# Kernel tuning notes

Hardware: AMD Instinct MI355X
Metric: run time of the kernel (lower is better)

Reference implementation:

```python
import jax, jax.numpy as jnp
import numpy as np

B, N, TASK_DIM, HW_DIM, EMB = 32768, 32, 17, 16, 64


def _w(key, shape, scale=0.1):
    return jax.random.normal(key, shape, dtype=jnp.float32) * scale


def setup_inputs() -> dict:
    key = jax.random.key(0)
    ks = jax.random.split(key, 24)
    inp = {
        "task_vecs": jax.random.normal(ks[0], (B, TASK_DIM), dtype=jnp.float32),
        "hw_vecs": jax.random.normal(ks[1], (B, N, HW_DIM), dtype=jnp.float32),
        "valid_mask": jnp.ones((B, N), dtype=bool),
        # TaskEncoder: Linear(17,64) ReLU Linear(64,64) ReLU
        "te_w1": _w(ks[2], (TASK_DIM, 64)), "te_b1": jnp.zeros((64,), jnp.float32),
        "te_w2": _w(ks[3], (64, EMB)),      "te_b2": jnp.zeros((EMB,), jnp.float32),
        # HWEncoder: Linear(16,64) ReLU Linear(64,64) ReLU
        "he_w1": _w(ks[4], (HW_DIM, 64)),   "he_b1": jnp.zeros((64,), jnp.float32),
        "he_w2": _w(ks[5], (64, EMB)),      "he_b2": jnp.zeros((EMB,), jnp.float32),
        # Scorer: Linear(128,64) ReLU Linear(64,32) ReLU Linear(32,1)
        "sc_w1": _w(ks[6], (2 * EMB, 64)),  "sc_b1": jnp.zeros((64,), jnp.float32),
        "sc_w2": _w(ks[7], (64, 32)),       "sc_b2": jnp.zeros((32,), jnp.float32),
        "sc_w3": _w(ks[8], (32, 1)),        "sc_b3": jnp.zeros((1,), jnp.float32),
        # RejectHead: Linear(64,32) ReLU Linear(32,1)
        "rj_w1": _w(ks[9], (EMB, 32)),      "rj_b1": jnp.zeros((32,), jnp.float32),
        "rj_w2": _w(ks[10], (32, 1)),       "rj_b2": jnp.zeros((1,), jnp.float32),
        # ValueHead: Linear(128,64) ReLU Linear(64,1)
        "vh_w1": _w(ks[11], (2 * EMB, 64)), "vh_b1": jnp.zeros((64,), jnp.float32),
        "vh_w2": _w(ks[12], (64, 1)),       "vh_b2": jnp.zeros((1,), jnp.float32),
    }
    return inp


def reference(task_vecs, hw_vecs, valid_mask,
              te_w1, te_b1, te_w2, te_b2,
              he_w1, he_b1, he_w2, he_b2,
              sc_w1, sc_b1, sc_w2, sc_b2, sc_w3, sc_b3,
              rj_w1, rj_b1, rj_w2, rj_b2,
              vh_w1, vh_b1, vh_w2, vh_b2):
    relu = jax.nn.relu
    # task embedding [B, EMB]
    task_emb = relu(relu(task_vecs @ te_w1 + te_b1) @ te_w2 + te_b2)
    # hw embeddings [B, N, EMB]
    hw_emb = relu(relu(hw_vecs @ he_w1 + he_b1) @ he_w2 + he_b2)
    # scorer on concat(task_emb, hw_emb) -> [B, N]
    comb = jnp.concatenate(
        [jnp.broadcast_to(task_emb[:, None, :], hw_emb.shape), hw_emb], axis=-1)
    h = relu(comb @ sc_w1 + sc_b1)
    h = relu(h @ sc_w2 + sc_b2)
    hw_scores = (h @ sc_w3 + sc_b3)[..., 0]  # [B, N]
    # reject score [B]
    reject = (relu(task_emb @ rj_w1 + rj_b1) @ rj_w2 + rj_b2)[..., 0]
    all_scores = jnp.concatenate([hw_scores, reject[:, None]], axis=1)  # [B, N+1]
    # mask (reject slot always valid)
    full_mask = jnp.concatenate(
        [valid_mask, jnp.ones((valid_mask.shape[0], 1), dtype=bool)], axis=1)
    all_scores = jnp.where(full_mask, all_scores, -jnp.inf)
    action_probs = jax.nn.softmax(all_scores, axis=1)
    # value head on concat(task_emb, mean hw_emb)
    mean_hw = hw_emb.mean(axis=1)
    vin = jnp.concatenate([task_emb, mean_hw], axis=1)
    value = (relu(vin @ vh_w1 + vh_b1) @ vh_w2 + vh_b2)[..., 0]  # [B]
    return action_probs, value, all_scores
```

## Files before the change

kernel.cpp:

```cpp
#include <hip/hip_runtime.h>
#include <hip/hip_bf16.h>

typedef __attribute__((ext_vector_type(8))) short bfrag;
typedef __attribute__((ext_vector_type(4))) float vf4;

#define MFMA16(A,B,C) __builtin_amdgcn_mfma_f32_16x16x32_bf16(A,B,C,0,0,0)

struct KParams {
  const float* task; const float* hw; const int* mask;
  const float* te_w1; const float* te_b1; const float* te_w2; const float* te_b2;
  const float* he_w1; const float* he_b1; const float* he_w2; const float* he_b2;
  const float* sc_w1; const float* sc_b1; const float* sc_w2; const float* sc_b2;
  const float* sc_w3; const float* sc_b3;
  const float* rj_w1; const float* rj_b1; const float* rj_w2; const float* rj_b2;
  const float* vh_w1; const float* vh_b1; const float* vh_w2; const float* vh_b2;
  float* out; float* ws; int B;
};

__device__ __forceinline__ unsigned pack2(float a, float b){
  __hip_bfloat162 h = __float22bfloat162_rn(make_float2(a,b));
  unsigned u; __builtin_memcpy(&u, &h, 4); return u;
}

__device__ __forceinline__ float frag_elem(const KParams& P, int fid, int lane, int e){
  const float* W; const float* bias = nullptr; int OUT = 64, KREAL, c, q = 0;
  if (fid < 4)       { W=P.te_w1; bias=P.te_b1; KREAL=17; c=fid; }
  else if (fid < 12) { W=P.te_w2;              KREAL=64; int t=fid-4;  c=t>>1; q=t&1; }
  else if (fid < 20) { W=P.sc_w1;              KREAL=64; int t=fid-12; c=t>>1; q=t&1; }
  else if (fid < 28) { W=P.vh_w1;              KREAL=64; int t=fid-20; c=t>>1; q=t&1; }
  else if (fid < 32) { W=P.rj_w1; OUT=32;      KREAL=64; int t=fid-28; c=t>>1; q=t&1; }
  else if (fid < 36) { W=P.he_w1; bias=P.he_b1; KREAL=16; c=fid-32; }
  else if (fid < 44) { W=P.he_w2;              KREAL=64; int t=fid-36; c=t>>1; q=t&1; }
  else if (fid < 52) { W=P.sc_w1 + 64*64;      KREAL=64; int t=fid-44; c=t>>1; q=t&1; }
  else if (fid < 56) { W=P.sc_w2; OUT=32;      KREAL=64; int t=fid-52; c=t>>1; q=t&1; }
  else               { W=P.vh_w1 + 64*64;      KREAL=64; int t=fid-56; c=t>>1; q=t&1; }
  int row = c*16 + (lane & 15);
  int k   = q*32 + ((e>>2)<<4) + ((lane>>4)<<2) + (e&3);
  if (k < KREAL) return W[k*OUT + row];
  if (k == KREAL && bias) return bias[row];
  return 0.f;
}

__device__ __forceinline__ float chunk_elem(const KParams& P, int cid, int lane, int r){
  const float* src; int base;
  if (cid < 4)       { src=P.te_b2; base=cid*16; }
  else if (cid < 8)  { src=P.sc_b1; base=(cid-4)*16; }
  else if (cid < 12) { src=P.vh_b1; base=(cid-8)*16; }
  else if (cid < 14) { src=P.rj_b1; base=(cid-12)*16; }
  else if (cid < 18) { src=P.he_b2; base=(cid-14)*16; }
  else if (cid < 20) { src=P.sc_b2; base=(cid-18)*16; }
  else if (cid < 22) { src=P.sc_w3; base=(cid-20)*16; }
  else if (cid < 24) { src=P.rj_w2; base=(cid-22)*16; }
  else               { src=P.vh_w2; base=(cid-24)*16; }
  return src[base + ((lane>>4)<<2) + r];
}

__global__ void setup_frags(KParams P){
  int l = threadIdx.x, bid = blockIdx.x;
  if (bid < 64){
    uint4 u;
    u.x = pack2(frag_elem(P,bid,l,0), frag_elem(P,bid,l,1));
    u.y = pack2(frag_elem(P,bid,l,2), frag_elem(P,bid,l,3));
    u.z = pack2(frag_elem(P,bid,l,4), frag_elem(P,bid,l,5));
    u.w = pack2(frag_elem(P,bid,l,6), frag_elem(P,bid,l,7));
    ((uint4*)P.ws)[bid*64 + l] = u;
  } else {
    int cid = bid - 64;
    float4 v;
    v.x = chunk_elem(P,cid,l,0); v.y = chunk_elem(P,cid,l,1);
    v.z = chunk_elem(P,cid,l,2); v.w = chunk_elem(P,cid,l,3);
    ((float4*)(P.ws + 16384))[cid*64 + l] = v;
  }
}

template<int WS>
__device__ __forceinline__ bfrag load_frag(const KParams& P, int fid, int l){
  union { uint4 q; bfrag v; } X;
  if (WS) X.q = ((const uint4*)P.ws)[fid*64 + l];
  else {
    X.q.x = pack2(frag_elem(P,fid,l,0), frag_elem(P,fid,l,1));
    X.q.y = pack2(frag_elem(P,fid,l,2), frag_elem(P,fid,l,3));
    X.q.z = pack2(frag_elem(P,fid,l,4), frag_elem(P,fid,l,5));
    X.q.w = pack2(frag_elem(P,fid,l,6), frag_elem(P,fid,l,7));
  }
  return X.v;
}
template<int WS>
__device__ __forceinline__ vf4 load_chunk(const KParams& P, int cid, int l){
  vf4 r;
  if (WS){
    float4 t = ((const float4*)(P.ws + 16384))[cid*64 + l];
    r[0]=t.x; r[1]=t.y; r[2]=t.z; r[3]=t.w;
  } else {
    r[0]=chunk_elem(P,cid,l,0); r[1]=chunk_elem(P,cid,l,1);
    r[2]=chunk_elem(P,cid,l,2); r[3]=chunk_elem(P,cid,l,3);
  }
  return r;
}

template<bool RELU>
__device__ __forceinline__ bfrag packAB(vf4 A, vf4 B){
  if (RELU){
    #pragma unroll
    for (int i=0;i<4;i++){ A[i]=fmaxf(A[i],0.f); B[i]=fmaxf(B[i],0.f); }
  }
  union { unsigned u[4]; bfrag v; } X;
  X.u[0]=pack2(A[0],A[1]); X.u[1]=pack2(A[2],A[3]);
  X.u[2]=pack2(B[0],B[1]); X.u[3]=pack2(B[2],B[3]);
  return X.v;
}

__device__ __forceinline__ bfrag ldsF(const uint4* lw, int j, int l){
  union { uint4 q; bfrag v; } X; X.q = lw[j*64 + l]; return X.v;
}

template<int WS>
__global__ __launch_bounds__(256,2) void fused_policy(KParams P){
  __shared__ uint4 lds_w[24*64];
  __shared__ float lds_sc[4][16][33];
  __shared__ float lds_pr[4][16][33];
  __shared__ float lds_inv[4][16];
  const int tid = threadIdx.x;
  const int wid = tid>>6, l = tid&63, col = l&15, grp = l>>4;
  const int b0  = (blockIdx.x*4 + wid)*16;
  const vf4 Z = {0.f,0.f,0.f,0.f};

  if (WS){
    const uint4* w4 = (const uint4*)P.ws;
    #pragma unroll
    for (int i=0;i<6;i++) lds_w[tid + i*256] = w4[32*64 + tid + i*256];
  } else {
    for (int i=tid; i<24*64; i+=256){
      int fid = 32 + (i>>6), lane = i&63;
      uint4 u;
      u.x = pack2(frag_elem(P,fid,lane,0), frag_elem(P,fid,lane,1));
      u.y = pack2(frag_elem(P,fid,lane,2), frag_elem(P,fid,lane,3));
      u.z = pack2(frag_elem(P,fid,lane,4), frag_elem(P,fid,lane,5));
      u.w = pack2(frag_elem(P,fid,lane,6), frag_elem(P,fid,lane,7));
      lds_w[i] = u;
    }
  }

  const float* tp = P.task + (size_t)(b0+col)*17;
  union { unsigned u[4]; bfrag v; } TB;
  TB.u[0]=pack2(tp[grp*4+0],tp[grp*4+1]);
  TB.u[1]=pack2(tp[grp*4+2],tp[grp*4+3]);
  TB.u[2]= (grp==0) ? pack2(tp[16], 1.f) : 0u;
  TB.u[3]=0u;
  vf4 a1[4];
  #pragma unroll
  for (int c=0;c<4;c++) a1[c] = MFMA16(load_frag<WS>(P,c,l), TB.v, Z);
  bfrag h1B0 = packAB<true>(a1[0],a1[1]), h1B1 = packAB<true>(a1[2],a1[3]);
  vf4 a2[4];
  #pragma unroll
  for (int c=0;c<4;c++){
    a2[c] = MFMA16(load_frag<WS>(P,4+2*c,l), h1B0, load_chunk<WS>(P,c,l));
    a2[c] = MFMA16(load_frag<WS>(P,5+2*c,l), h1B1, a2[c]);
  }
  bfrag teB0 = packAB<true>(a2[0],a2[1]), teB1 = packAB<true>(a2[2],a2[3]);
  vf4 tc[4];
  #pragma unroll
  for (int c=0;c<4;c++){
    tc[c] = MFMA16(load_frag<WS>(P,12+2*c,l), teB0, load_chunk<WS>(P,4+c,l));
    tc[c] = MFMA16(load_frag<WS>(P,13+2*c,l), teB1, tc[c]);
  }
  vf4 vc[4];
  #pragma unroll
  for (int c=0;c<4;c++){
    vc[c] = MFMA16(load_frag<WS>(P,20+2*c,l), teB0, load_chunk<WS>(P,8+c,l));
    vc[c] = MFMA16(load_frag<WS>(P,21+2*c,l), teB1, vc[c]);
  }
  float rpart = 0.f;
  #pragma unroll
  for (int c=0;c<2;c++){
    vf4 rv = MFMA16(load_frag<WS>(P,28+2*c,l), teB0, load_chunk<WS>(P,12+c,l));
    rv = MFMA16(load_frag<WS>(P,29+2*c,l), teB1, rv);
    vf4 w2 = load_chunk<WS>(P,22+c,l);
    #pragma unroll
    for (int r=0;r<4;r++) rpart += fmaxf(rv[r],0.f)*w2[r];
  }
  rpart += __shfl_xor(rpart,16);
  rpart += __shfl_xor(rpart,32);
  const float reject = rpart + P.rj_b2[0];

  vf4 Bhe2[4], Bsc2[2], W3[2];
  #pragma unroll
  for (int c=0;c<4;c++) Bhe2[c]=load_chunk<WS>(P,14+c,l);
  #pragma unroll
  for (int c=0;c<2;c++) Bsc2[c]=load_chunk<WS>(P,18+c,l);
  #pragma unroll
  for (int c=0;c<2;c++) W3[c]=load_chunk<WS>(P,20+c,l);
  const float scb3 = P.sc_b3[0];
  vf4 macc[4];
  #pragma unroll
  for (int c=0;c<4;c++) macc[c]=Z;

  __syncthreads();

  const float* hwp = P.hw + (size_t)(b0+col)*512 + grp*4;
  float4 hvA = *(const float4*)(hwp);
  float4 hvB = *(const float4*)(hwp + 16);
  #pragma unroll 1
  for (int n=0;n<32;n+=2){
    float4 nA = hvA, nB = hvB;
    if (n < 30){
      nA = *(const float4*)(hwp + (n+2)*16);
      nB = *(const float4*)(hwp + (n+3)*16);
    }
    union { unsigned u[4]; bfrag v; } H0, H1;
    H0.u[0]=pack2(hvA.x,hvA.y); H0.u[1]=pack2(hvA.z,hvA.w);
    H0.u[2]= (grp==0) ? pack2(1.f,0.f) : 0u;
    H0.u[3]=0u;
    H1.u[0]=pack2(hvB.x,hvB.y); H1.u[1]=pack2(hvB.z,hvB.w);
    H1.u[2]=H0.u[2]; H1.u[3]=0u;

    vf4 g1a[4], g1b[4];
    #pragma unroll
    for (int c=0;c<4;c++){
      bfrag f = ldsF(lds_w, c, l);
      g1a[c]=MFMA16(f, H0.v, Z);
      g1b[c]=MFMA16(f, H1.v, Z);
    }
    bfrag g1aB0 = packAB<true>(g1a[0],g1a[1]), g1aB1 = packAB<true>(g1a[2],g1a[3]);
    bfrag g1bB0 = packAB<true>(g1b[0],g1b[1]), g1bB1 = packAB<true>(g1b[2],g1b[3]);

    vf4 g2a[4], g2b[4];
    #pragma unroll
    for (int c=0;c<4;c++){
      bfrag f0 = ldsF(lds_w, 4+2*c, l), f1 = ldsF(lds_w, 5+2*c, l);
      g2a[c]=MFMA16(f1, g1aB1, MFMA16(f0, g1aB0, Bhe2[c]));
      g2b[c]=MFMA16(f1, g1bB1, MFMA16(f0, g1bB0, Bhe2[c]));
      #pragma unroll
      for (int r=0;r<4;r++){
        g2a[c][r]=fmaxf(g2a[c][r],0.f); g2b[c][r]=fmaxf(g2b[c][r],0.f);
        macc[c][r] += g2a[c][r] + g2b[c][r];
      }
    }
    bfrag g2aB0 = packAB<false>(g2a[0],g2a[1]), g2aB1 = packAB<false>(g2a[2],g2a[3]);
    bfrag g2bB0 = packAB<false>(g2b[0],g2b[1]), g2bB1 = packAB<false>(g2b[2],g2b[3]);

    vf4 s1a[4], s1b[4];
    #pragma unroll
    for (int c=0;c<4;c++){
      bfrag f0 = ldsF(lds_w, 12+2*c, l), f1 = ldsF(lds_w, 13+2*c, l);
      s1a[c]=MFMA16(f1, g2aB1, MFMA16(f0, g2aB0, tc[c]));
      s1b[c]=MFMA16(f1, g2bB1, MFMA16(f0, g2bB0, tc[c]));
    }
    bfrag s1aB0 = packAB<true>(s1a[0],s1a[1]), s1aB1 = packAB<true>(s1a[2],s1a[3]);
    bfrag s1bB0 = packAB<true>(s1b[0],s1b[1]), s1bB1 = packAB<true>(s1b[2],s1b[3]);

    float sp0 = 0.f, sp1 = 0.f;
    #pragma unroll
    for (int c=0;c<2;c++){
      bfrag f0 = ldsF(lds_w, 20+2*c, l), f1 = ldsF(lds_w, 21+2*c, l);
      vf4 s2a = MFMA16(f1, s1aB1, MFMA16(f0, s1aB0, Bsc2[c]));
      vf4 s2b = MFMA16(f1, s1bB1, MFMA16(f0, s1bB0, Bsc2[c]));
      #pragma unroll
      for (int r=0;r<4;r++){
        sp0 += fmaxf(s2a[r],0.f)*W3[c][r];
        sp1 += fmaxf(s2b[r],0.f)*W3[c][r];
      }
    }
    sp0 += __shfl_xor(sp0,16); sp0 += __shfl_xor(sp0,32);
    sp1 += __shfl_xor(sp1,16); sp1 += __shfl_xor(sp1,32);
    if (l<16){
      lds_sc[wid][l][n]   = sp0 + scb3;
      lds_sc[wid][l][n+1] = sp1 + scb3;
    }
    hvA = nA; hvB = nB;
  }
  if (l<16) lds_sc[wid][l][32] = reject;

  #pragma unroll
  for (int c=0;c<4;c++){
    #pragma unroll
    for (int r=0;r<4;r++) macc[c][r] *= (1.f/32.f);
  }
  bfrag mB0 = packAB<false>(macc[0],macc[1]), mB1 = packAB<false>(macc[2],macc[3]);
  float vpart = 0.f;
  #pragma unroll
  for (int c=0;c<4;c++){
    vf4 vD = MFMA16(load_frag<WS>(P,56+2*c,l), mB0, vc[c]);
    vD     = MFMA16(load_frag<WS>(P,57+2*c,l), mB1, vD);
    vf4 w2 = load_chunk<WS>(P,24+c,l);
    #pragma unroll
    for (int r=0;r<4;r++) vpart += fmaxf(vD[r],0.f)*w2[r];
  }
  vpart += __shfl_xor(vpart,16);
  vpart += __shfl_xor(vpart,32);
  if (l<16) P.out[(size_t)P.B*33 + b0 + l] = vpart + P.vh_b2[0];

  asm volatile("s_waitcnt lgkmcnt(0)" ::: "memory");
  if (l<16){
    float s[33];
    #pragma unroll
    for (int j=0;j<32;j++) s[j]=lds_sc[wid][l][j];
    s[32]=reject;
    const int4* mp = (const int4*)(P.mask + (size_t)(b0+l)*32);
    #pragma unroll
    for (int w=0;w<8;w++){
      int4 m4 = mp[w];
      if (m4.x==0) s[w*4+0] = -INFINITY;
      if (m4.y==0) s[w*4+1] = -INFINITY;
      if (m4.z==0) s[w*4+2] = -INFINITY;
      if (m4.w==0) s[w*4+3] = -INFINITY;
    }
    #pragma unroll
    for (int j=0;j<32;j++) lds_sc[wid][l][j] = s[j];
    float mx = s[32];
    #pragma unroll
    for (int j=0;j<32;j++) mx = fmaxf(mx, s[j]);
    float sum = 0.f;
    #pragma unroll
    for (int j=0;j<33;j++){
      float p = __expf(s[j]-mx); sum += p; lds_pr[wid][l][j] = p;
    }
    lds_inv[wid][l] = 1.f/sum;
  }
  asm volatile("s_waitcnt lgkmcnt(0)" ::: "memory");
  const float* prf = &lds_pr[wid][0][0];
  const float* scf = &lds_sc[wid][0][0];
  #pragma unroll 1
  for (int i=l; i<528; i+=64){
    unsigned bl = (unsigned)i/33u;
    P.out[(size_t)b0*33 + i]                      = prf[i]*lds_inv[wid][bl];
    P.out[(size_t)P.B*34 + (size_t)b0*33 + i]     = scf[i];
  }
}

extern "C" void kernel_launch(void* const* d_in, const int* in_sizes, int n_in,
                              void* d_out, int out_size, void* d_ws, size_t ws_size,
                              hipStream_t stream){
  KParams P;
  P.task  = (const float*)d_in[0];
  P.hw    = (const float*)d_in[1];
  P.mask  = (const int*)d_in[2];
  P.te_w1 = (const float*)d_in[3];  P.te_b1 = (const float*)d_in[4];
  P.te_w2 = (const float*)d_in[5];  P.te_b2 = (const float*)d_in[6];
  P.he_w1 = (const float*)d_in[7];  P.he_b1 = (const float*)d_in[8];
  P.he_w2 = (const float*)d_in[9];  P.he_b2 = (const float*)d_in[10];
  P.sc_w1 = (const float*)d_in[11]; P.sc_b1 = (const float*)d_in[12];
  P.sc_w2 = (const float*)d_in[13]; P.sc_b2 = (const float*)d_in[14];
  P.sc_w3 = (const float*)d_in[15]; P.sc_b3 = (const float*)d_in[16];
  P.rj_w1 = (const float*)d_in[17]; P.rj_b1 = (const float*)d_in[18];
  P.rj_w2 = (const float*)d_in[19]; P.rj_b2 = (const float*)d_in[20];
  P.vh_w1 = (const float*)d_in[21]; P.vh_b1 = (const float*)d_in[22];
  P.vh_w2 = (const float*)d_in[23]; P.vh_b2 = (const float*)d_in[24];
  P.out = (float*)d_out;
  P.ws  = (float*)d_ws;
  P.B   = in_sizes[0] / 17;
  const size_t need = 64u*1024u + 28u*1024u;
  const bool use_ws = (d_ws != nullptr) && (ws_size >= need);
  if (use_ws){
    setup_frags<<<92, 64, 0, stream>>>(P);
    fused_policy<1><<<P.B/64, 256, 0, stream>>>(P);
  } else {
    fused_policy<0><<<P.B/64, 256, 0, stream>>>(P);
  }
}
```

Baseline: 59.82 us.

## Split hardware-slot loop across two waves per batch tile and fast bf16 pack

Doubles the block to 512 threads so two waves share each 16-row batch tile, each processing half of the 32 hardware slots. Mean-embedding partials are combined through LDS, then one wave computes the value head while the other does masking, softmax and output stores. Separately, float-to-bf16 packing becomes an add-and-permute rounding trick that does not handle NaN. The change adds per-tile work duplication (task encoder in both waves) and extra block barriers in exchange for more parallelism and shorter per-wave latency.

```diff
diff --git a/kernel.cpp b/kernel.cpp
--- a/kernel.cpp
+++ b/kernel.cpp
@@ -18,8 +18,10 @@
 };
 
 __device__ __forceinline__ unsigned pack2(float a, float b){
-  __hip_bfloat162 h = __float22bfloat162_rn(make_float2(a,b));
-  unsigned u; __builtin_memcpy(&u, &h, 4); return u;
+  unsigned ua, ub;
+  __builtin_memcpy(&ua, &a, 4);
+  __builtin_memcpy(&ub, &b, 4);
+  return __builtin_amdgcn_perm(ub + 0x8000u, ua + 0x8000u, 0x07060302u);
 }
 
 __device__ __forceinline__ float frag_elem(const KParams& P, int fid, int lane, int e){
@@ -115,22 +117,24 @@
 }
 
 template<int WS>
-__global__ __launch_bounds__(256,2) void fused_policy(KParams P){
+__global__ __launch_bounds__(512,3) void fused_policy(KParams P){
   __shared__ uint4 lds_w[24*64];
   __shared__ float lds_sc[4][16][33];
   __shared__ float lds_pr[4][16][33];
+  __shared__ float lds_mc[4][64][16];
   __shared__ float lds_inv[4][16];
   const int tid = threadIdx.x;
   const int wid = tid>>6, l = tid&63, col = l&15, grp = l>>4;
-  const int b0  = (blockIdx.x*4 + wid)*16;
+  const int pair = wid & 3, half = wid >> 2;
+  const int b0  = (blockIdx.x*4 + pair)*16;
   const vf4 Z = {0.f,0.f,0.f,0.f};
 
   if (WS){
     const uint4* w4 = (const uint4*)P.ws;
     #pragma unroll
-    for (int i=0;i<6;i++) lds_w[tid + i*256] = w4[32*64 + tid + i*256];
-  } else {
-    for (int i=tid; i<24*64; i+=256){
+    for (int i=0;i<3;i++) lds_w[tid + i*512] = w4[32*64 + tid + i*512];
+  } else {
+    for (int i=tid; i<24*64; i+=512){
       int fid = 32 + (i>>6), lane = i&63;
       uint4 u;
       u.x = pack2(frag_elem(P,fid,lane,0), frag_elem(P,fid,lane,1));
@@ -164,12 +168,6 @@
     tc[c] = MFMA16(load_frag<WS>(P,12+2*c,l), teB0, load_chunk<WS>(P,4+c,l));
     tc[c] = MFMA16(load_frag<WS>(P,13+2*c,l), teB1, tc[c]);
   }
-  vf4 vc[4];
-  #pragma unroll
-  for (int c=0;c<4;c++){
-    vc[c] = MFMA16(load_frag<WS>(P,20+2*c,l), teB0, load_chunk<WS>(P,8+c,l));
-    vc[c] = MFMA16(load_frag<WS>(P,21+2*c,l), teB1, vc[c]);
-  }
   float rpart = 0.f;
   #pragma unroll
   for (int c=0;c<2;c++){
@@ -197,15 +195,15 @@
 
   __syncthreads();
 
-  const float* hwp = P.hw + (size_t)(b0+col)*512 + grp*4;
+  const float* hwp = P.hw + (size_t)(b0+col)*512 + half*256 + grp*4;
   float4 hvA = *(const float4*)(hwp);
   float4 hvB = *(const float4*)(hwp + 16);
   #pragma unroll 1
-  for (int n=0;n<32;n+=2){
+  for (int i=0;i<8;i++){
     float4 nA = hvA, nB = hvB;
-    if (n < 30){
-      nA = *(const float4*)(hwp + (n+2)*16);
-      nB = *(const float4*)(hwp + (n+3)*16);
+    if (i < 7){
+      nA = *(const float4*)(hwp + (2*i+2)*16);
+      nB = *(const float4*)(hwp + (2*i+3)*16);
     }
     union { unsigned u[4]; bfrag v; } H0, H1;
     H0.u[0]=pack2(hvA.x,hvA.y); H0.u[1]=pack2(hvA.z,hvA.w);
@@ -264,67 +262,84 @@
     sp0 += __shfl_xor(sp0,16); sp0 += __shfl_xor(sp0,32);
     sp1 += __shfl_xor(sp1,16); sp1 += __shfl_xor(sp1,32);
     if (l<16){
-      lds_sc[wid][l][n]   = sp0 + scb3;
-      lds_sc[wid][l][n+1] = sp1 + scb3;
+      lds_sc[pair][l][half*16 + 2*i]     = sp0 + scb3;
+      lds_sc[pair][l][half*16 + 2*i + 1] = sp1 + scb3;
     }
     hvA = nA; hvB = nB;
   }
-  if (l<16) lds_sc[wid][l][32] = reject;
-
-  #pragma unroll
-  for (int c=0;c<4;c++){
-    #pragma unroll
-    for (int r=0;r<4;r++) macc[c][r] *= (1.f/32.f);
-  }
-  bfrag mB0 = packAB<false>(macc[0],macc[1]), mB1 = packAB<false>(macc[2],macc[3]);
-  float vpart = 0.f;
-  #pragma unroll
-  for (int c=0;c<4;c++){
-    vf4 vD = MFMA16(load_frag<WS>(P,56+2*c,l), mB0, vc[c]);
-    vD     = MFMA16(load_frag<WS>(P,57+2*c,l), mB1, vD);
-    vf4 w2 = load_chunk<WS>(P,24+c,l);
-    #pragma unroll
-    for (int r=0;r<4;r++) vpart += fmaxf(vD[r],0.f)*w2[r];
-  }
-  vpart += __shfl_xor(vpart,16);
-  vpart += __shfl_xor(vpart,32);
-  if (l<16) P.out[(size_t)P.B*33 + b0 + l] = vpart + P.vh_b2[0];
-
-  asm volatile("s_waitcnt lgkmcnt(0)" ::: "memory");
-  if (l<16){
-    float s[33];
-    #pragma unroll
-    for (int j=0;j<32;j++) s[j]=lds_sc[wid][l][j];
-    s[32]=reject;
-    const int4* mp = (const int4*)(P.mask + (size_t)(b0+l)*32);
-    #pragma unroll
-    for (int w=0;w<8;w++){
-      int4 m4 = mp[w];
-      if (m4.x==0) s[w*4+0] = -INFINITY;
-      if (m4.y==0) s[w*4+1] = -INFINITY;
-      if (m4.z==0) s[w*4+2] = -INFINITY;
-      if (m4.w==0) s[w*4+3] = -INFINITY;
-    }
-    #pragma unroll
-    for (int j=0;j<32;j++) lds_sc[wid][l][j] = s[j];
-    float mx = s[32];
-    #pragma unroll
-    for (int j=0;j<32;j++) mx = fmaxf(mx, s[j]);
-    float sum = 0.f;
-    #pragma unroll
-    for (int j=0;j<33;j++){
-      float p = __expf(s[j]-mx); sum += p; lds_pr[wid][l][j] = p;
-    }
-    lds_inv[wid][l] = 1.f/sum;
-  }
-  asm volatile("s_waitcnt lgkmcnt(0)" ::: "memory");
-  const float* prf = &lds_pr[wid][0][0];
-  const float* scf = &lds_sc[wid][0][0];
-  #pragma unroll 1
-  for (int i=l; i<528; i+=64){
-    unsigned bl = (unsigned)i/33u;
-    P.out[(size_t)b0*33 + i]                      = prf[i]*lds_inv[wid][bl];
-    P.out[(size_t)P.B*34 + (size_t)b0*33 + i]     = scf[i];
+
+  __syncthreads();
+
+  if (half==0){
+    #pragma unroll
+    for (int c=0;c<4;c++)
+      *(float4*)&lds_mc[pair][l][c*4] = make_float4(macc[c][0],macc[c][1],macc[c][2],macc[c][3]);
+    if (l<16) lds_sc[pair][l][32] = reject;
+  }
+  __syncthreads();
+
+  if (half==1){
+    vf4 vc[4];
+    #pragma unroll
+    for (int c=0;c<4;c++){
+      vc[c] = MFMA16(load_frag<WS>(P,20+2*c,l), teB0, load_chunk<WS>(P,8+c,l));
+      vc[c] = MFMA16(load_frag<WS>(P,21+2*c,l), teB1, vc[c]);
+    }
+    #pragma unroll
+    for (int c=0;c<4;c++){
+      float4 pm = *(const float4*)&lds_mc[pair][l][c*4];
+      macc[c][0]=(macc[c][0]+pm.x)*(1.f/32.f); macc[c][1]=(macc[c][1]+pm.y)*(1.f/32.f);
+      macc[c][2]=(macc[c][2]+pm.z)*(1.f/32.f); macc[c][3]=(macc[c][3]+pm.w)*(1.f/32.f);
+    }
+    bfrag mB0 = packAB<false>(macc[0],macc[1]), mB1 = packAB<false>(macc[2],macc[3]);
+    float vpart = 0.f;
+    #pragma unroll
+    for (int c=0;c<4;c++){
+      vf4 vD = MFMA16(load_frag<WS>(P,56+2*c,l), mB0, vc[c]);
+      vD     = MFMA16(load_frag<WS>(P,57+2*c,l), mB1, vD);
+      vf4 w2 = load_chunk<WS>(P,24+c,l);
+      #pragma unroll
+      for (int r=0;r<4;r++) vpart += fmaxf(vD[r],0.f)*w2[r];
+    }
+    vpart += __shfl_xor(vpart,16);
+    vpart += __shfl_xor(vpart,32);
+    if (l<16) P.out[(size_t)P.B*33 + b0 + l] = vpart + P.vh_b2[0];
+  } else {
+    if (l<16){
+      float s[33];
+      #pragma unroll
+      for (int j=0;j<32;j++) s[j]=lds_sc[pair][l][j];
+      s[32]=reject;
+      const int4* mp = (const int4*)(P.mask + (size_t)(b0+l)*32);
+      #pragma unroll
+      for (int w=0;w<8;w++){
+        int4 m4 = mp[w];
+        if (m4.x==0) s[w*4+0] = -INFINITY;
+        if (m4.y==0) s[w*4+1] = -INFINITY;
+        if (m4.z==0) s[w*4+2] = -INFINITY;
+        if (m4.w==0) s[w*4+3] = -INFINITY;
+      }
+      #pragma unroll
+      for (int j=0;j<32;j++) lds_sc[pair][l][j] = s[j];
+      float mx = s[32];
+      #pragma unroll
+      for (int j=0;j<32;j++) mx = fmaxf(mx, s[j]);
+      float sum = 0.f;
+      #pragma unroll
+      for (int j=0;j<33;j++){
+        float p = __expf(s[j]-mx); sum += p; lds_pr[pair][l][j] = p;
+      }
+      lds_inv[pair][l] = 1.f/sum;
+    }
+    asm volatile("s_waitcnt lgkmcnt(0)" ::: "memory");
+    const float* prf = &lds_pr[pair][0][0];
+    const float* scf = &lds_sc[pair][0][0];
+    #pragma unroll 1
+    for (int i=l; i<528; i+=64){
+      unsigned bl = (unsigned)i/33u;
+      P.out[(size_t)b0*33 + i]                      = prf[i]*lds_inv[pair][bl];
+      P.out[(size_t)P.B*34 + (size_t)b0*33 + i]     = scf[i];
+    }
   }
 }
 
@@ -353,8 +368,8 @@
   const bool use_ws = (d_ws != nullptr) && (ws_size >= need);
   if (use_ws){
     setup_frags<<<92, 64, 0, stream>>>(P);
-    fused_policy<1><<<P.B/64, 256, 0, stream>>>(P);
-  } else {
-    fused_policy<0><<<P.B/64, 256, 0, stream>>>(P);
-  }
-}
+    fused_policy<1><<<P.B/64, 512, 0, stream>>>(P);
+  } else {
+    fused_policy<0><<<P.B/64, 512, 0, stream>>>(P);
+  }
+}
```

Result: slower. 181.0 us (+202.6%).
